# Performance work log

Measured on AMD Instinct MI355X. Metric: run time of the kernel, lower is better.

The kernel has to match this reference:

```python
import jax, jax.numpy as jnp
import numpy as np

# dimensions
B, NQ, D, H, L, KT, KF = 4, 8192, 256, 8, 4, 2, 2
K = KT * KF
DH = D // H
SPATIAL = np.array([[64, 64], [32, 32], [16, 16], [8, 8]], dtype=np.int32)  # (H_l, W_l)
_sizes = SPATIAL[:, 0] * SPATIAL[:, 1]
LSI = np.concatenate([[0], np.cumsum(_sizes)[:-1]]).astype(np.int32)
NV = int(_sizes.sum())


def setup_inputs() -> dict:
    key = jax.random.key(0)
    ks = jax.random.split(key, 12)
    s = 0.02  # small weight scale keeps tanh in linear region like the zero-init original
    # biases per _reset_parameters: +-0.5 grid for offsets, level-specialization for level_weights
    b_time = jnp.asarray(np.tile(np.linspace(-0.5, 0.5, KT), H * L).astype(np.float32))
    b_freq = jnp.asarray(np.tile(np.linspace(-0.5, 0.5, KF).astype(np.float32), H * L))
    lvl_bias = np.zeros((H, L), dtype=np.float32)
    hpl = max(1, H // L)
    for lvl in range(L):
        lvl_bias[lvl * hpl:min(lvl * hpl + hpl, H), lvl] = 1.0
    return dict(
        query=jax.random.normal(ks[0], (B, NQ, D), jnp.float32),
        reference_points=jax.random.uniform(ks[1], (B, NQ, L, 2), jnp.float32),
        value=jax.random.normal(ks[2], (B, NV, D), jnp.float32),
        spatial_shapes=jnp.asarray(SPATIAL),
        level_start_index=jnp.asarray(LSI),
        W_time=jax.random.normal(ks[3], (D, H * L * KT), jnp.float32) * s,
        b_time=b_time,
        W_freq=jax.random.normal(ks[4], (D, H * L * KF), jnp.float32) * s,
        b_freq=b_freq,
        W_lvl=jax.random.normal(ks[5], (D, H * L), jnp.float32) * s,
        b_lvl=jnp.asarray(lvl_bias.reshape(-1)),
        W_pt=jax.random.normal(ks[6], (D, H * L * K), jnp.float32) * s,
        b_pt=jnp.zeros((H * L * K,), jnp.float32),
        W_v=jax.random.normal(ks[7], (D, D), jnp.float32) * (1.0 / np.sqrt(D)),
        b_v=jnp.zeros((D,), jnp.float32),
        W_o=jax.random.normal(ks[8], (D, D), jnp.float32) * (1.0 / np.sqrt(D)),
        b_o=jnp.zeros((D,), jnp.float32),
    )


def _bilinear(vlev, gx, gy, Hl, Wl):
    # vlev: [B,H,Hl*Wl,DH]; gx,gy: [B,H,NQ,K] normalized grid coords in [-1,1]
    # F.grid_sample(align_corners=False, padding_mode='zeros') semantics
    x = (gx + 1.0) * (Wl * 0.5) - 0.5
    y = (gy + 1.0) * (Hl * 0.5) - 0.5
    x0 = jnp.floor(x)
    y0 = jnp.floor(y)
    wx1 = x - x0
    wy1 = y - y0
    x0i = x0.astype(jnp.int32)
    y0i = y0.astype(jnp.int32)

    def gather(xi, yi, w):
        valid = (xi >= 0) & (xi < Wl) & (yi >= 0) & (yi < Hl)
        idx = jnp.clip(yi, 0, Hl - 1) * Wl + jnp.clip(xi, 0, Wl - 1)
        b, h, nq, k = idx.shape
        v = jnp.take_along_axis(vlev, idx.reshape(b, h, nq * k)[..., None], axis=2)
        v = v.reshape(b, h, nq, k, DH)
        return v * (w * valid)[..., None]

    return (gather(x0i, y0i, (1.0 - wx1) * (1.0 - wy1))
            + gather(x0i + 1, y0i, wx1 * (1.0 - wy1))
            + gather(x0i, y0i + 1, (1.0 - wx1) * wy1)
            + gather(x0i + 1, y0i + 1, wx1 * wy1))


def _forward(query, reference_points, value, W_time, b_time, W_freq, b_freq,
             W_lvl, b_lvl, W_pt, b_pt, W_v, b_v, W_o, b_o,
             spatial_shapes, level_start_index):
    ss = np.asarray(spatial_shapes)
    lsi = np.asarray(level_start_index)
    # predicted separable offsets (offset_scale = 1.0)
    t_off = jnp.tanh(query @ W_time + b_time).reshape(B, NQ, H, L, KT)
    f_off = jnp.tanh(query @ W_freq + b_freq).reshape(B, NQ, H, L, KF)
    # square grid: outer product of time (x) and freq (y) offsets -> K = KT*KF points
    off = jnp.stack([
        jnp.broadcast_to(t_off[..., :, None], (B, NQ, H, L, KT, KF)),
        jnp.broadcast_to(f_off[..., None, :], (B, NQ, H, L, KT, KF)),
    ], axis=-1).reshape(B, NQ, H, L, K, 2)
    # normalizer: (W_l, H_l) per level
    norm = jnp.stack([spatial_shapes[:, 1], spatial_shapes[:, 0]], axis=-1).astype(jnp.float32)
    loc = reference_points[:, :, None, :, None, :] + off / norm[None, None, None, :, None, :]
    loc = jnp.clip(loc, 0.0, 1.0)
    grid = 2.0 * loc - 1.0  # [B,NQ,H,L,K,2], last dim = (x, y)
    # attention weights: softmax over levels times softmax over points
    lw = jax.nn.softmax((query @ W_lvl + b_lvl).reshape(B, NQ, H, L), axis=-1)
    pw = jax.nn.softmax((query @ W_pt + b_pt).reshape(B, NQ, H, L, K), axis=-1)
    attn = lw[..., None] * pw  # [B,NQ,H,L,K]
    v = (value @ W_v + b_v).reshape(B, NV, H, DH)
    out = jnp.zeros((B, NQ, H, DH), jnp.float32)
    for lid in range(L):
        Hl, Wl = int(ss[lid, 0]), int(ss[lid, 1])
        start = int(lsi[lid])
        vlev = v[:, start:start + Hl * Wl].transpose(0, 2, 1, 3)  # [B,H,S_l,DH]
        gx = grid[:, :, :, lid, :, 0].transpose(0, 2, 1, 3)  # [B,H,NQ,K]
        gy = grid[:, :, :, lid, :, 1].transpose(0, 2, 1, 3)
        sampled = _bilinear(vlev, gx, gy, Hl, Wl)  # [B,H,NQ,K,DH]
        a = attn[:, :, :, lid, :].transpose(0, 2, 1, 3)  # [B,H,NQ,K]
        out = out + jnp.einsum('bhqkd,bhqk->bqhd', sampled, a)
    out = out.reshape(B, NQ, D)
    return out @ W_o + b_o


def reference(query, reference_points, value, spatial_shapes, level_start_index,
              W_time, b_time, W_freq, b_freq, W_lvl, b_lvl, W_pt, b_pt,
              W_v, b_v, W_o, b_o):
    return _forward(query, reference_points, value, W_time, b_time, W_freq, b_freq,
                    W_lvl, b_lvl, W_pt, b_pt, W_v, b_v, W_o, b_o,
                    spatial_shapes, level_start_index)
```

## Files before the change

### kernel.cpp

```cpp
#include <hip/hip_runtime.h>
#include <math.h>

#define B_  4
#define NQ_ 8192
#define D_  256
#define H_  8
#define L_  4
#define K_  4
#define DH_ 32
#define NV_ 5440

#define SLAB_ 5936

typedef short bf16x8 __attribute__((ext_vector_type(8)));
typedef float f32x4  __attribute__((ext_vector_type(4)));
typedef float f32x8  __attribute__((ext_vector_type(8)));
typedef unsigned short u16x8 __attribute__((ext_vector_type(8)));

__device__ __forceinline__ ushort f2bf(float f) {
    union { float f; unsigned u; } v; v.f = f;
    return (ushort)((v.u + 0x7FFF + ((v.u >> 16) & 1)) >> 16);
}
__device__ __forceinline__ float bf2f(ushort u) {
    union { unsigned u; float f; } v; v.u = ((unsigned)u) << 16;
    return v.f;
}
__device__ __forceinline__ void gld16(const void* g, void* l) {
    __builtin_amdgcn_global_load_lds(
        (const __attribute__((address_space(1))) unsigned int*)g,
        (__attribute__((address_space(3))) unsigned int*)l, 16, 0, 0);
}

__global__ __launch_bounds__(256) void k_prep(const float* __restrict__ Wv,
                                              const float* __restrict__ Wo,
                                              const float* __restrict__ Wt,
                                              const float* __restrict__ Wf,
                                              const float* __restrict__ Wlv,
                                              const float* __restrict__ Wp,
                                              uint4* __restrict__ vzero,
                                              ushort* __restrict__ Wvt,
                                              ushort* __restrict__ Wot,
                                              ushort* __restrict__ Wqt) {
    const int bk = blockIdx.x;
    const int t  = threadIdx.x;
    if (bk < 2968) {
        vzero[(size_t)bk * 256 + t] = make_uint4(0, 0, 0, 0);
    } else if (bk < 3480) {
        const float* in; ushort* out; int n;
        if (bk < 3224) { in = Wv; out = Wvt; n = bk - 2968; }
        else           { in = Wo; out = Wot; n = bk - 3224; }
        out[n * 256 + t] = f2bf(in[t * 256 + n]);
    } else {
        const int n = bk - 3480;
        float v;
        if (n < 64)       v = Wt[t * 64 + n];
        else if (n < 128) v = Wf[t * 64 + (n - 64)];
        else if (n < 160) v = Wlv[t * 32 + (n - 128)];
        else              v = Wp[t * 128 + (n - 160)];
        Wqt[n * 256 + t] = f2bf(v);
    }
}

template<int MODE, int AF32>
__global__ __launch_bounds__(256) void k_gemm(const void* __restrict__ Ap,
                                              const ushort* __restrict__ Bt,
                                              const float* __restrict__ bias,
                                              void* __restrict__ Cp) {
    __shared__ __align__(16) ushort As[2][128 * 32];
    __shared__ __align__(16) ushort Bs[2][128 * 32];
    const int m0   = blockIdx.x * 128;
    const int n0   = blockIdx.y * 128;
    const int t    = threadIdx.x;
    const int w    = t >> 6;
    const int lane = t & 63;
    const int wm   = (w >> 1) * 64;
    const int wn   = (w & 1) * 64;
    const int lm   = lane & 15;
    const int quad = lane >> 4;

    float4 areg[4];

    auto stageB = [&](int buf, int kc) {
        #pragma unroll
        for (int i = 0; i < 2; ++i) {
            const int c0 = (i * 4 + w) * 64;
            const int c  = c0 + lane;
            const int row = c >> 2, ko = (c & 3) * 8;
            gld16(&Bt[(size_t)(n0 + row) * 256 + kc + ko],
                  (ushort*)&Bs[buf][0] + (size_t)c0 * 8);
        }
    };
    auto stageA16 = [&](int buf, int kc) {
        const ushort* A = (const ushort*)Ap;
        #pragma unroll
        for (int i = 0; i < 2; ++i) {
            const int c0 = (i * 4 + w) * 64;
            const int c  = c0 + lane;
            const int row = c >> 2, ko = (c & 3) * 8;
            gld16(&A[(size_t)(m0 + row) * 256 + kc + ko],
                  (ushort*)&As[buf][0] + (size_t)c0 * 8);
        }
    };
    auto loadA32 = [&](int kc) {
        const float* A = (const float*)Ap;
        #pragma unroll
        for (int i = 0; i < 4; ++i) {
            const int c = t + i * 256;
            const int row = c >> 3, ko = (c & 7) * 4;
            areg[i] = *(const float4*)&A[(size_t)(m0 + row) * 256 + kc + ko];
        }
    };
    auto writeA32 = [&](int buf) {
        #pragma unroll
        for (int i = 0; i < 4; ++i) {
            const int c = t + i * 256;
            const int row = c >> 3, ko = (c & 7) * 4;
            ushort4 u;
            u.x = f2bf(areg[i].x); u.y = f2bf(areg[i].y);
            u.z = f2bf(areg[i].z); u.w = f2bf(areg[i].w);
            *(ushort4*)&As[buf][row * 32 + ko] = u;
        }
    };

    f32x4 acc[4][4];
    #pragma unroll
    for (int i = 0; i < 4; ++i)
        #pragma unroll
        for (int j = 0; j < 4; ++j)
            acc[i][j] = (f32x4)(0.f);

    if (AF32) { loadA32(0); writeA32(0); }
    else      { stageA16(0, 0); }
    stageB(0, 0);
    __syncthreads();

    int cur = 0;
    for (int kc = 0; kc < 256; kc += 32) {
        const int nxt = cur ^ 1;
        bf16x8 af[4], bfr[4];
        #pragma unroll
        for (int mf = 0; mf < 4; ++mf)
            af[mf] = *(const bf16x8*)&As[cur][(wm + mf * 16 + lm) * 32 + quad * 8];
        #pragma unroll
        for (int nf = 0; nf < 4; ++nf)
            bfr[nf] = *(const bf16x8*)&Bs[cur][(wn + nf * 16 + lm) * 32 + quad * 8];
        if (kc + 32 < 256) {
            if (AF32) loadA32(kc + 32);
            else      stageA16(nxt, kc + 32);
            stageB(nxt, kc + 32);
        }
        #pragma unroll
        for (int mf = 0; mf < 4; ++mf)
            #pragma unroll
            for (int nf = 0; nf < 4; ++nf)
                acc[mf][nf] = __builtin_amdgcn_mfma_f32_16x16x32_bf16(
                    af[mf], bfr[nf], acc[mf][nf], 0, 0, 0);
        if (kc + 32 < 256) {
            if (AF32) writeA32(nxt);
            __syncthreads();
        }
        cur = nxt;
    }

    #pragma unroll
    for (int mf = 0; mf < 4; ++mf) {
        #pragma unroll
        for (int nf = 0; nf < 4; ++nf) {
            const f32x4 a = acc[mf][nf];
            const int col   = n0 + wn + nf * 16 + lm;
            const int rbase = m0 + wm + mf * 16 + quad * 4;
            #pragma unroll
            for (int r = 0; r < 4; ++r) {
                const int row = rbase + r;
                const float v = a[r];
                if (MODE == 0) {
                    ((float*)Cp)[(size_t)row * 256 + col] = v + bias[col];
                } else {
                    const int b = row / NV_, s = row - b * NV_;
                    const int h = col >> 5, dh = col & 31;
                    const int l = (s >= 5376) ? 3 : (s >= 5120) ? 2 : (s >= 4096) ? 1 : 0;
                    const int lsi_[4] = {0, 4096, 5120, 5376};
                    const int po_[4]  = {0, 4356, 5512, 5836};
                    const int o  = s - lsi_[l];
                    const int Wl = 64 >> l;
                    const int y  = o >> (6 - l);
                    const int x  = o & (Wl - 1);
                    const int prow = po_[l] + (y + 1) * (Wl + 2) + (x + 1);
                    ((ushort*)Cp)[(((size_t)(b * H_ + h)) * SLAB_ + prow) * 32 + dh] =
                        f2bf(v + bias[col]);
                }
            }
        }
    }
}

__global__ __launch_bounds__(256) void k_qproj(const float* __restrict__ query,
                                               const ushort* __restrict__ Wqt,
                                               const float* __restrict__ refpts,
                                               const float* __restrict__ bt,
                                               const float* __restrict__ bfq,
                                               const float* __restrict__ blv,
                                               const float* __restrict__ bp,
                                               float* __restrict__ params) {
    __shared__ __align__(16) char smem[45056];
    ushort* As0 = (ushort*)smem;
    ushort* Bs0 = (ushort*)(smem + 8192);
    float*  ep  = (float*)smem;

    const int m0   = blockIdx.x * 64;
    const int t    = threadIdx.x;
    const int w    = t >> 6;
    const int lane = t & 63;
    const int wm   = (w >> 1) * 32;
    const int wn   = (w & 1) * 144;
    const int lm   = lane & 15;
    const int quad = lane >> 4;

    float4 areg[2];

    auto stageB = [&](int buf, int kc) {
        ushort* B = Bs0 + buf * 9216;
        #pragma unroll
        for (int i = 0; i < 5; ++i) {
            const int cb = i * 4 + w;
            if (cb < 18) {
                const int c0 = cb * 64;
                const int c  = c0 + lane;
                const int row = c >> 2, ko = (c & 3) * 8;
                gld16(&Wqt[(size_t)row * 256 + kc + ko], B + (size_t)c0 * 8);
            }
        }
    };
    auto loadA = [&](int kc) {
        #pragma unroll
        for (int i = 0; i < 2; ++i) {
            const int c = t + i * 256;
            const int row = c >> 3, ko = (c & 7) * 4;
            areg[i] = *(const float4*)&query[(size_t)(m0 + row) * 256 + kc + ko];
        }
    };
    auto writeA = [&](int buf) {
        ushort* A = As0 + buf * 2048;
        #pragma unroll
        for (int i = 0; i < 2; ++i) {
            const int c = t + i * 256;
            const int row = c >> 3, ko = (c & 7) * 4;
            ushort4 u;
            u.x = f2bf(areg[i].x); u.y = f2bf(areg[i].y);
            u.z = f2bf(areg[i].z); u.w = f2bf(areg[i].w);
            *(ushort4*)&A[row * 32 + ko] = u;
        }
    };

    f32x4 acc[2][9];
    #pragma unroll
    for (int i = 0; i < 2; ++i)
        #pragma unroll
        for (int j = 0; j < 9; ++j)
            acc[i][j] = (f32x4)(0.f);

    loadA(0); writeA(0);
    stageB(0, 0);
    __syncthreads();

    int cur = 0;
    for (int kc = 0; kc < 256; kc += 32) {
        const int nxt = cur ^ 1;
        const ushort* Ac = As0 + cur * 2048;
        const ushort* Bc = Bs0 + cur * 9216;
        bf16x8 af[2], bfr[9];
        #pragma unroll
        for (int mf = 0; mf < 2; ++mf)
            af[mf] = *(const bf16x8*)&Ac[(wm + mf * 16 + lm) * 32 + quad * 8];
        #pragma unroll
        for (int nf = 0; nf < 9; ++nf)
            bfr[nf] = *(const bf16x8*)&Bc[(wn + nf * 16 + lm) * 32 + quad * 8];
        if (kc + 32 < 256) {
            loadA(kc + 32);
            stageB(nxt, kc + 32);
        }
        #pragma unroll
        for (int mf = 0; mf < 2; ++mf)
            #pragma unroll
            for (int nf = 0; nf < 9; ++nf)
                acc[mf][nf] = __builtin_amdgcn_mfma_f32_16x16x32_bf16(
                    af[mf], bfr[nf], acc[mf][nf], 0, 0, 0);
        if (kc + 32 < 256) {
            writeA(nxt);
            __syncthreads();
        }
        cur = nxt;
    }

    #pragma unroll
    for (int ph = 0; ph < 2; ++ph) {
        __syncthreads();
        if ((w >> 1) == ph) {
            #pragma unroll
            for (int mf = 0; mf < 2; ++mf)
                #pragma unroll
                for (int nf = 0; nf < 9; ++nf)
                    #pragma unroll
                    for (int r = 0; r < 4; ++r)
                        ep[(mf * 16 + quad * 4 + r) * 296 + wn + nf * 16 + lm]
                            = acc[mf][nf][r];
        }
        __syncthreads();
        #pragma unroll
        for (int it = 0; it < 4; ++it) {
            const int item = t + it * 256;
            const int qr = item >> 5;
            const int hl = item & 31;
            const int h = hl >> 2, l = hl & 3;
            const int qg = m0 + ph * 32 + qr;
            const float* lgr = &ep[qr * 296];

            const float tA = tanhf(lgr[hl * 2 + 0] + bt[hl * 2 + 0]);
            const float tB = tanhf(lgr[hl * 2 + 1] + bt[hl * 2 + 1]);
            const float fA = tanhf(lgr[64 + hl * 2 + 0] + bfq[hl * 2 + 0]);
            const float fB = tanhf(lgr[64 + hl * 2 + 1] + bfq[hl * 2 + 1]);

            const float l0 = lgr[128 + h * 4 + 0] + blv[h * 4 + 0];
            const float l1 = lgr[128 + h * 4 + 1] + blv[h * 4 + 1];
            const float l2 = lgr[128 + h * 4 + 2] + blv[h * 4 + 2];
            const float l3 = lgr[128 + h * 4 + 3] + blv[h * 4 + 3];
            const float lmx = fmaxf(fmaxf(l0, l1), fmaxf(l2, l3));
            const float e0 = __expf(l0 - lmx), e1 = __expf(l1 - lmx);
            const float e2 = __expf(l2 - lmx), e3 = __expf(l3 - lmx);
            const float lsum = e0 + e1 + e2 + e3;
            const float lwv = ((l == 0) ? e0 : (l == 1) ? e1 : (l == 2) ? e2 : e3) / lsum;

            const float p0 = lgr[160 + hl * 4 + 0] + bp[hl * 4 + 0];
            const float p1 = lgr[160 + hl * 4 + 1] + bp[hl * 4 + 1];
            const float p2 = lgr[160 + hl * 4 + 2] + bp[hl * 4 + 2];
            const float p3 = lgr[160 + hl * 4 + 3] + bp[hl * 4 + 3];
            const float pmx = fmaxf(fmaxf(p0, p1), fmaxf(p2, p3));
            const float q0e = __expf(p0 - pmx), q1e = __expf(p1 - pmx);
            const float q2e = __expf(p2 - pmx), q3e = __expf(p3 - pmx);
            const float inv = lwv / (q0e + q1e + q2e + q3e);

            const float rx = refpts[((size_t)qg * L_ + l) * 2 + 0];
            const float ry = refpts[((size_t)qg * L_ + l) * 2 + 1];
            const float Wlf = (float)(64 >> l);
            const float Hlf = (float)(64 >> l);
            const float xA = fminf(fmaxf(rx + tA / Wlf, 0.f), 1.f) * Wlf - 0.5f;
            const float xB = fminf(fmaxf(rx + tB / Wlf, 0.f), 1.f) * Wlf - 0.5f;
            const float yA = fminf(fmaxf(ry + fA / Hlf, 0.f), 1.f) * Hlf - 0.5f;
            const float yB = fminf(fmaxf(ry + fB / Hlf, 0.f), 1.f) * Hlf - 0.5f;

            float* pp = params + (size_t)qg * 256 + hl * 8;
            pp[0] = q0e * inv; pp[1] = q1e * inv; pp[2] = q2e * inv; pp[3] = q3e * inv;
            pp[4] = xA; pp[5] = xB; pp[6] = yA; pp[7] = yB;
        }
    }
}

__global__ __launch_bounds__(256) void k_sample(const ushort* __restrict__ vperm,
                                                const float* __restrict__ params,
                                                ushort* __restrict__ mid) {
    __shared__ float pm[8][264];
    const int fid = blockIdx.x;
    const int b   = (fid & 7) >> 1;
    const int q0  = (((fid >> 3) << 1) | (fid & 1)) * 8;
    const int t   = threadIdx.x;
    const int ql  = t >> 5;
    const int sub = t & 31;
    const int h   = sub >> 2;
    const int dh8 = sub & 3;

    for (int i = t; i < 8 * 256; i += 256) {
        const int q = i >> 8, c = i & 255;
        pm[q][(c >> 5) * 33 + (c & 31)] = params[((size_t)(b * NQ_ + q0 + q)) * 256 + c];
    }
    __syncthreads();

    const ushort* vb = vperm + ((size_t)(b * H_ + h)) * SLAB_ * 32 + dh8 * 8;
    const int po_[4] = {0, 4356, 5512, 5836};

    f32x8 acc = (f32x8)(0.f);
    #pragma unroll
    for (int l = 0; l < L_; ++l) {
        const int W2 = (64 >> l) + 2;
        const ushort* vl = vb + (size_t)po_[l] * 32;
        const float* p  = &pm[ql][h * 33 + l * 8];
        const float a0 = p[0], a1 = p[1], a2 = p[2], a3 = p[3];
        const float xA = p[4], xB = p[5], yA = p[6], yB = p[7];
        const float xa0 = floorf(xA), xb0 = floorf(xB);
        const float ya0 = floorf(yA), yb0 = floorf(yB);
        const float fxa = xA - xa0, fxb = xB - xb0;
        const float fya = yA - ya0, fyb = yB - yb0;
        const int pxa = (int)xa0 + 1, pxb = (int)xb0 + 1;
        const int pya = (int)ya0 + 1, pyb = (int)yb0 + 1;
        #pragma unroll
        for (int k = 0; k < 4; ++k) {
            const int   px = (k & 2) ? pxb : pxa;
            const int   py = (k & 1) ? pyb : pya;
            const float fx = (k & 2) ? fxb : fxa;
            const float fy = (k & 1) ? fyb : fya;
            const float ak = (k == 0) ? a0 : (k == 1) ? a1 : (k == 2) ? a2 : a3;
            const ushort* cp = vl + (size_t)(py * W2 + px) * 32;
            const u16x8 u00 = *(const u16x8*)cp;
            const u16x8 u10 = *(const u16x8*)(cp + 32);
            const u16x8 u01 = *(const u16x8*)(cp + W2 * 32);
            const u16x8 u11 = *(const u16x8*)(cp + (W2 + 1) * 32);
            const float gx = 1.f - fx, gy = 1.f - fy;
            const float w00 = ak * gx * gy, w10 = ak * fx * gy;
            const float w01 = ak * gx * fy, w11 = ak * fx * fy;
            #pragma unroll
            for (int e = 0; e < 8; ++e)
                acc[e] += bf2f(u00[e]) * w00 + bf2f(u10[e]) * w10
                        + bf2f(u01[e]) * w01 + bf2f(u11[e]) * w11;
        }
    }
    u16x8 o;
    #pragma unroll
    for (int e = 0; e < 8; ++e) o[e] = f2bf(acc[e]);
    *(u16x8*)&mid[((size_t)(b * NQ_ + q0 + ql)) * 256 + sub * 8] = o;
}

extern "C" void kernel_launch(void* const* d_in, const int* in_sizes, int n_in,
                              void* d_out, int out_size, void* d_ws, size_t ws_size,
                              hipStream_t stream) {
    const float* query = (const float*)d_in[0];
    const float* refp  = (const float*)d_in[1];
    const float* value = (const float*)d_in[2];
    const float* Wt = (const float*)d_in[5];
    const float* bt = (const float*)d_in[6];
    const float* Wf = (const float*)d_in[7];
    const float* bf = (const float*)d_in[8];
    const float* Wl = (const float*)d_in[9];
    const float* bl = (const float*)d_in[10];
    const float* Wp = (const float*)d_in[11];
    const float* bp = (const float*)d_in[12];
    const float* Wv = (const float*)d_in[13];
    const float* bv = (const float*)d_in[14];
    const float* Wo = (const float*)d_in[15];
    const float* bo = (const float*)d_in[16];

    char* wsb = (char*)d_ws;
    ushort* vperm  = (ushort*)wsb;
    float*  params = (float*)(wsb + 12156928);
    ushort* midb   = (ushort*)(wsb + 45711360);
    ushort* Wvt    = (ushort*)(wsb + 62488576);
    ushort* Wot    = (ushort*)(wsb + 62619648);
    ushort* Wqt    = (ushort*)(wsb + 62750720);

    k_prep<<<3768, 256, 0, stream>>>(Wv, Wo, Wt, Wf, Wl, Wp,
                                     (uint4*)vperm, Wvt, Wot, Wqt);
    k_gemm<1, 1><<<dim3(170, 2), 256, 0, stream>>>(value, Wvt, bv, vperm);
    k_qproj<<<512, 256, 0, stream>>>(query, Wqt, refp, bt, bf, bl, bp, params);
    k_sample<<<dim3(NQ_ / 8 * B_), 256, 0, stream>>>(vperm, params, midb);
    k_gemm<0, 0><<<dim3(256, 2), 256, 0, stream>>>(midb, Wot, bo, (float*)d_out);
}
```

Before: 222.4 us.

## Fuse value and query projections into one launch; zero only slab borders

Merges the value projection GEMM, the query projection/param kernel and a new border-zeroing role into a single heterogeneous launch selected by block index. The full memset of the padded value slab in the prep kernel is replaced by writing zeros only to the one-element border ring of each padded level, since the interior is overwritten by the projection. This removes a kernel launch, lets the two independent projections share the GPU concurrently, and cuts the zero-fill traffic. It relies on the border enumeration exactly covering every padded cell the sampler can read, and the fused kernel's occupancy is now bounded by the larger shared-memory footprint.

```diff
diff --git a/kernel.cpp b/kernel.cpp
--- a/kernel.cpp
+++ b/kernel.cpp
@@ -37,21 +37,18 @@
                                               const float* __restrict__ Wf,
                                               const float* __restrict__ Wlv,
                                               const float* __restrict__ Wp,
-                                              uint4* __restrict__ vzero,
                                               ushort* __restrict__ Wvt,
                                               ushort* __restrict__ Wot,
                                               ushort* __restrict__ Wqt) {
     const int bk = blockIdx.x;
     const int t  = threadIdx.x;
-    if (bk < 2968) {
-        vzero[(size_t)bk * 256 + t] = make_uint4(0, 0, 0, 0);
-    } else if (bk < 3480) {
+    if (bk < 512) {
         const float* in; ushort* out; int n;
-        if (bk < 3224) { in = Wv; out = Wvt; n = bk - 2968; }
-        else           { in = Wo; out = Wot; n = bk - 3224; }
+        if (bk < 256) { in = Wv; out = Wvt; n = bk; }
+        else          { in = Wo; out = Wot; n = bk - 256; }
         out[n * 256 + t] = f2bf(in[t * 256 + n]);
     } else {
-        const int n = bk - 3480;
+        const int n = bk - 512;
         float v;
         if (n < 64)       v = Wt[t * 64 + n];
         else if (n < 128) v = Wf[t * 64 + (n - 64)];
@@ -61,11 +58,339 @@
     }
 }
 
-template<int MODE, int AF32>
-__global__ __launch_bounds__(256) void k_gemm(const void* __restrict__ Ap,
-                                              const ushort* __restrict__ Bt,
-                                              const float* __restrict__ bias,
-                                              void* __restrict__ Cp) {
+__device__ __forceinline__ void vproj_role(char* smem, int fid,
+                                           const float* __restrict__ value,
+                                           const ushort* __restrict__ Wvt,
+                                           const float* __restrict__ bv,
+                                           ushort* __restrict__ vperm) {
+    ushort* As0 = (ushort*)smem;
+    ushort* Bs0 = (ushort*)(smem + 16384);
+    const int m0   = (fid % 170) * 128;
+    const int n0   = (fid / 170) * 128;
+    const int t    = threadIdx.x;
+    const int w    = t >> 6;
+    const int lane = t & 63;
+    const int wm   = (w >> 1) * 64;
+    const int wn   = (w & 1) * 64;
+    const int lm   = lane & 15;
+    const int quad = lane >> 4;
+
+    float4 areg[4];
+
+    auto stageB = [&](int buf, int kc) {
+        ushort* B = Bs0 + buf * 4096;
+        #pragma unroll
+        for (int i = 0; i < 2; ++i) {
+            const int c0 = (i * 4 + w) * 64;
+            const int c  = c0 + lane;
+            const int row = c >> 2, ko = (c & 3) * 8;
+            gld16(&Wvt[(size_t)(n0 + row) * 256 + kc + ko], B + (size_t)c0 * 8);
+        }
+    };
+    auto loadA = [&](int kc) {
+        #pragma unroll
+        for (int i = 0; i < 4; ++i) {
+            const int c = t + i * 256;
+            const int row = c >> 3, ko = (c & 7) * 4;
+            areg[i] = *(const float4*)&value[(size_t)(m0 + row) * 256 + kc + ko];
+        }
+    };
+    auto writeA = [&](int buf) {
+        ushort* A = As0 + buf * 4096;
+        #pragma unroll
+        for (int i = 0; i < 4; ++i) {
+            const int c = t + i * 256;
+            const int row = c >> 3, ko = (c & 7) * 4;
+            ushort4 u;
+            u.x = f2bf(areg[i].x); u.y = f2bf(areg[i].y);
+            u.z = f2bf(areg[i].z); u.w = f2bf(areg[i].w);
+            *(ushort4*)&A[row * 32 + ko] = u;
+        }
+    };
+
+    f32x4 acc[4][4];
+    #pragma unroll
+    for (int i = 0; i < 4; ++i)
+        #pragma unroll
+        for (int j = 0; j < 4; ++j)
+            acc[i][j] = (f32x4)(0.f);
+
+    loadA(0); writeA(0);
+    stageB(0, 0);
+    __syncthreads();
+
+    int cur = 0;
+    for (int kc = 0; kc < 256; kc += 32) {
+        const int nxt = cur ^ 1;
+        const ushort* Ac = As0 + cur * 4096;
+        const ushort* Bc = Bs0 + cur * 4096;
+        bf16x8 af[4], bfr[4];
+        #pragma unroll
+        for (int mf = 0; mf < 4; ++mf)
+            af[mf] = *(const bf16x8*)&Ac[(wm + mf * 16 + lm) * 32 + quad * 8];
+        #pragma unroll
+        for (int nf = 0; nf < 4; ++nf)
+            bfr[nf] = *(const bf16x8*)&Bc[(wn + nf * 16 + lm) * 32 + quad * 8];
+        if (kc + 32 < 256) {
+            loadA(kc + 32);
+            stageB(nxt, kc + 32);
+        }
+        #pragma unroll
+        for (int mf = 0; mf < 4; ++mf)
+            #pragma unroll
+            for (int nf = 0; nf < 4; ++nf)
+                acc[mf][nf] = __builtin_amdgcn_mfma_f32_16x16x32_bf16(
+                    af[mf], bfr[nf], acc[mf][nf], 0, 0, 0);
+        if (kc + 32 < 256) {
+            writeA(nxt);
+            __syncthreads();
+        }
+        cur = nxt;
+    }
+
+    #pragma unroll
+    for (int mf = 0; mf < 4; ++mf) {
+        #pragma unroll
+        for (int nf = 0; nf < 4; ++nf) {
+            const f32x4 a = acc[mf][nf];
+            const int col   = n0 + wn + nf * 16 + lm;
+            const int rbase = m0 + wm + mf * 16 + quad * 4;
+            #pragma unroll
+            for (int r = 0; r < 4; ++r) {
+                const int row = rbase + r;
+                const float v = a[r];
+                const int b = row / NV_, s = row - b * NV_;
+                const int h = col >> 5, dh = col & 31;
+                const int l = (s >= 5376) ? 3 : (s >= 5120) ? 2 : (s >= 4096) ? 1 : 0;
+                const int lsi_[4] = {0, 4096, 5120, 5376};
+                const int po_[4]  = {0, 4356, 5512, 5836};
+                const int o  = s - lsi_[l];
+                const int Wl = 64 >> l;
+                const int y  = o >> (6 - l);
+                const int x  = o & (Wl - 1);
+                const int prow = po_[l] + (y + 1) * (Wl + 2) + (x + 1);
+                vperm[(((size_t)(b * H_ + h)) * SLAB_ + prow) * 32 + dh] =
+                    f2bf(v + bv[col]);
+            }
+        }
+    }
+}
+
+__device__ __forceinline__ void qproj_role(char* smem, int fid,
+                                           const float* __restrict__ query,
+                                           const ushort* __restrict__ Wqt,
+                                           const float* __restrict__ refpts,
+                                           const float* __restrict__ bt,
+                                           const float* __restrict__ bfq,
+                                           const float* __restrict__ blv,
+                                           const float* __restrict__ bp,
+                                           float* __restrict__ params) {
+    ushort* As0 = (ushort*)smem;
+    ushort* Bs0 = (ushort*)(smem + 8192);
+    float*  ep  = (float*)smem;
+
+    const int m0   = fid * 64;
+    const int t    = threadIdx.x;
+    const int w    = t >> 6;
+    const int lane = t & 63;
+    const int wm   = (w >> 1) * 32;
+    const int wn   = (w & 1) * 144;
+    const int lm   = lane & 15;
+    const int quad = lane >> 4;
+
+    float4 areg[2];
+
+    auto stageB = [&](int buf, int kc) {
+        ushort* B = Bs0 + buf * 9216;
+        #pragma unroll
+        for (int i = 0; i < 5; ++i) {
+            const int cb = i * 4 + w;
+            if (cb < 18) {
+                const int c0 = cb * 64;
+                const int c  = c0 + lane;
+                const int row = c >> 2, ko = (c & 3) * 8;
+                gld16(&Wqt[(size_t)row * 256 + kc + ko], B + (size_t)c0 * 8);
+            }
+        }
+    };
+    auto loadA = [&](int kc) {
+        #pragma unroll
+        for (int i = 0; i < 2; ++i) {
+            const int c = t + i * 256;
+            const int row = c >> 3, ko = (c & 7) * 4;
+            areg[i] = *(const float4*)&query[(size_t)(m0 + row) * 256 + kc + ko];
+        }
+    };
+    auto writeA = [&](int buf) {
+        ushort* A = As0 + buf * 2048;
+        #pragma unroll
+        for (int i = 0; i < 2; ++i) {
+            const int c = t + i * 256;
+            const int row = c >> 3, ko = (c & 7) * 4;
+            ushort4 u;
+            u.x = f2bf(areg[i].x); u.y = f2bf(areg[i].y);
+            u.z = f2bf(areg[i].z); u.w = f2bf(areg[i].w);
+            *(ushort4*)&A[row * 32 + ko] = u;
+        }
+    };
+
+    f32x4 acc[2][9];
+    #pragma unroll
+    for (int i = 0; i < 2; ++i)
+        #pragma unroll
+        for (int j = 0; j < 9; ++j)
+            acc[i][j] = (f32x4)(0.f);
+
+    loadA(0); writeA(0);
+    stageB(0, 0);
+    __syncthreads();
+
+    int cur = 0;
+    for (int kc = 0; kc < 256; kc += 32) {
+        const int nxt = cur ^ 1;
+        const ushort* Ac = As0 + cur * 2048;
+        const ushort* Bc = Bs0 + cur * 9216;
+        bf16x8 af[2], bfr[9];
+        #pragma unroll
+        for (int mf = 0; mf < 2; ++mf)
+            af[mf] = *(const bf16x8*)&Ac[(wm + mf * 16 + lm) * 32 + quad * 8];
+        #pragma unroll
+        for (int nf = 0; nf < 9; ++nf)
+            bfr[nf] = *(const bf16x8*)&Bc[(wn + nf * 16 + lm) * 32 + quad * 8];
+        if (kc + 32 < 256) {
+            loadA(kc + 32);
+            stageB(nxt, kc + 32);
+        }
+        #pragma unroll
+        for (int mf = 0; mf < 2; ++mf)
+            #pragma unroll
+            for (int nf = 0; nf < 9; ++nf)
+                acc[mf][nf] = __builtin_amdgcn_mfma_f32_16x16x32_bf16(
+                    af[mf], bfr[nf], acc[mf][nf], 0, 0, 0);
+        if (kc + 32 < 256) {
+            writeA(nxt);
+            __syncthreads();
+        }
+        cur = nxt;
+    }
+
+    #pragma unroll
+    for (int ph = 0; ph < 2; ++ph) {
+        __syncthreads();
+        if ((w >> 1) == ph) {
+            #pragma unroll
+            for (int mf = 0; mf < 2; ++mf)
+                #pragma unroll
+                for (int nf = 0; nf < 9; ++nf)
+                    #pragma unroll
+                    for (int r = 0; r < 4; ++r)
+                        ep[(mf * 16 + quad * 4 + r) * 296 + wn + nf * 16 + lm]
+                            = acc[mf][nf][r];
+        }
+        __syncthreads();
+        #pragma unroll
+        for (int it = 0; it < 4; ++it) {
+            const int item = t + it * 256;
+            const int qr = item >> 5;
+            const int hl = item & 31;
+            const int h = hl >> 2, l = hl & 3;
+            const int qg = m0 + ph * 32 + qr;
+            const float* lgr = &ep[qr * 296];
+
+            const float tA = tanhf(lgr[hl * 2 + 0] + bt[hl * 2 + 0]);
+            const float tB = tanhf(lgr[hl * 2 + 1] + bt[hl * 2 + 1]);
+            const float fA = tanhf(lgr[64 + hl * 2 + 0] + bfq[hl * 2 + 0]);
+            const float fB = tanhf(lgr[64 + hl * 2 + 1] + bfq[hl * 2 + 1]);
+
+            const float l0 = lgr[128 + h * 4 + 0] + blv[h * 4 + 0];
+            const float l1 = lgr[128 + h * 4 + 1] + blv[h * 4 + 1];
+            const float l2 = lgr[128 + h * 4 + 2] + blv[h * 4 + 2];
+            const float l3 = lgr[128 + h * 4 + 3] + blv[h * 4 + 3];
+            const float lmx = fmaxf(fmaxf(l0, l1), fmaxf(l2, l3));
+            const float e0 = __expf(l0 - lmx), e1 = __expf(l1 - lmx);
+            const float e2 = __expf(l2 - lmx), e3 = __expf(l3 - lmx);
+            const float lsum = e0 + e1 + e2 + e3;
+            const float lwv = ((l == 0) ? e0 : (l == 1) ? e1 : (l == 2) ? e2 : e3) / lsum;
+
+            const float p0 = lgr[160 + hl * 4 + 0] + bp[hl * 4 + 0];
+            const float p1 = lgr[160 + hl * 4 + 1] + bp[hl * 4 + 1];
+            const float p2 = lgr[160 + hl * 4 + 2] + bp[hl * 4 + 2];
+            const float p3 = lgr[160 + hl * 4 + 3] + bp[hl * 4 + 3];
+            const float pmx = fmaxf(fmaxf(p0, p1), fmaxf(p2, p3));
+            const float q0e = __expf(p0 - pmx), q1e = __expf(p1 - pmx);
+            const float q2e = __expf(p2 - pmx), q3e = __expf(p3 - pmx);
+            const float inv = lwv / (q0e + q1e + q2e + q3e);
+
+            const float rx = refpts[((size_t)qg * L_ + l) * 2 + 0];
+            const float ry = refpts[((size_t)qg * L_ + l) * 2 + 1];
+            const float Wlf = (float)(64 >> l);
+            const float Hlf = (float)(64 >> l);
+            const float xA = fminf(fmaxf(rx + tA / Wlf, 0.f), 1.f) * Wlf - 0.5f;
+            const float xB = fminf(fmaxf(rx + tB / Wlf, 0.f), 1.f) * Wlf - 0.5f;
+            const float yA = fminf(fmaxf(ry + fA / Hlf, 0.f), 1.f) * Hlf - 0.5f;
+            const float yB = fminf(fmaxf(ry + fB / Hlf, 0.f), 1.f) * Hlf - 0.5f;
+
+            float* pp = params + (size_t)qg * 256 + hl * 8;
+            pp[0] = q0e * inv; pp[1] = q1e * inv; pp[2] = q2e * inv; pp[3] = q3e * inv;
+            pp[4] = xA; pp[5] = xB; pp[6] = yA; pp[7] = yB;
+        }
+    }
+}
+
+__device__ __forceinline__ void border_role(int fid, ushort* __restrict__ vperm) {
+    const int t = threadIdx.x;
+    const int p = fid * 256 + t;
+    const int bh = p / 496;
+    int e = p - bh * 496;
+    int l = 0;
+    if (e >= 460)      { l = 3; e -= 460; }
+    else if (e >= 392) { l = 2; e -= 392; }
+    else if (e >= 260) { l = 1; e -= 260; }
+    const int po_[4] = {0, 4356, 5512, 5836};
+    const int W2 = (64 >> l) + 2;
+    int row, col;
+    if (e < 2 * W2) {
+        row = (e < W2) ? 0 : (W2 - 1);
+        col = (e < W2) ? e : (e - W2);
+    } else {
+        const int e2 = e - 2 * W2;
+        row = 1 + (e2 >> 1);
+        col = (e2 & 1) ? (W2 - 1) : 0;
+    }
+    uint4* dst = (uint4*)&vperm[((size_t)bh * SLAB_ + po_[l] + row * W2 + col) * 32];
+    dst[0] = make_uint4(0, 0, 0, 0);
+    dst[1] = make_uint4(0, 0, 0, 0);
+    dst[2] = make_uint4(0, 0, 0, 0);
+    dst[3] = make_uint4(0, 0, 0, 0);
+}
+
+__global__ __launch_bounds__(256) void k_fused(const float* __restrict__ value,
+                                               const ushort* __restrict__ Wvt,
+                                               const float* __restrict__ bv,
+                                               ushort* __restrict__ vperm,
+                                               const float* __restrict__ query,
+                                               const ushort* __restrict__ Wqt,
+                                               const float* __restrict__ refpts,
+                                               const float* __restrict__ bt,
+                                               const float* __restrict__ bfq,
+                                               const float* __restrict__ blv,
+                                               const float* __restrict__ bp,
+                                               float* __restrict__ params) {
+    __shared__ __align__(16) char smem[45056];
+    const int fid = blockIdx.x;
+    if (fid < 340) {
+        vproj_role(smem, fid, value, Wvt, bv, vperm);
+    } else if (fid < 852) {
+        qproj_role(smem, fid - 340, query, Wqt, refpts, bt, bfq, blv, bp, params);
+    } else {
+        border_role(fid - 852, vperm);
+    }
+}
+
+__global__ __launch_bounds__(256) void k_ogemm(const ushort* __restrict__ A,
+                                               const ushort* __restrict__ Bt,
+                                               const float* __restrict__ bias,
+                                               float* __restrict__ Cp) {
     __shared__ __align__(16) ushort As[2][128 * 32];
     __shared__ __align__(16) ushort Bs[2][128 * 32];
     const int m0   = blockIdx.x * 128;
@@ -78,47 +403,13 @@
     const int lm   = lane & 15;
     const int quad = lane >> 4;
 
-    float4 areg[4];
-
-    auto stageB = [&](int buf, int kc) {
+    auto stage = [&](ushort* dst, const ushort* src, int row0, int kc) {
         #pragma unroll
         for (int i = 0; i < 2; ++i) {
             const int c0 = (i * 4 + w) * 64;
             const int c  = c0 + lane;
             const int row = c >> 2, ko = (c & 3) * 8;
-            gld16(&Bt[(size_t)(n0 + row) * 256 + kc + ko],
-                  (ushort*)&Bs[buf][0] + (size_t)c0 * 8);
-        }
-    };
-    auto stageA16 = [&](int buf, int kc) {
-        const ushort* A = (const ushort*)Ap;
-        #pragma unroll
-        for (int i = 0; i < 2; ++i) {
-            const int c0 = (i * 4 + w) * 64;
-            const int c  = c0 + lane;
-            const int row = c >> 2, ko = (c & 3) * 8;
-            gld16(&A[(size_t)(m0 + row) * 256 + kc + ko],
-                  (ushort*)&As[buf][0] + (size_t)c0 * 8);
-        }
-    };
-    auto loadA32 = [&](int kc) {
-        const float* A = (const float*)Ap;
-        #pragma unroll
-        for (int i = 0; i < 4; ++i) {
-            const int c = t + i * 256;
-            const int row = c >> 3, ko = (c & 7) * 4;
-            areg[i] = *(const float4*)&A[(size_t)(m0 + row) * 256 + kc + ko];
-        }
-    };
-    auto writeA32 = [&](int buf) {
-        #pragma unroll
-        for (int i = 0; i < 4; ++i) {
-            const int c = t + i * 256;
-            const int row = c >> 3, ko = (c & 7) * 4;
-            ushort4 u;
-            u.x = f2bf(areg[i].x); u.y = f2bf(areg[i].y);
-            u.z = f2bf(areg[i].z); u.w = f2bf(areg[i].w);
-            *(ushort4*)&As[buf][row * 32 + ko] = u;
+            gld16(&src[(size_t)(row0 + row) * 256 + kc + ko], dst + (size_t)c0 * 8);
         }
     };
 
@@ -129,9 +420,8 @@
         for (int j = 0; j < 4; ++j)
             acc[i][j] = (f32x4)(0.f);
 
-    if (AF32) { loadA32(0); writeA32(0); }
-    else      { stageA16(0, 0); }
-    stageB(0, 0);
+    stage(&As[0][0], A, m0, 0);
+    stage(&Bs[0][0], Bt, n0, 0);
     __syncthreads();
 
     int cur = 0;
@@ -145,9 +435,8 @@
         for (int nf = 0; nf < 4; ++nf)
             bfr[nf] = *(const bf16x8*)&Bs[cur][(wn + nf * 16 + lm) * 32 + quad * 8];
         if (kc + 32 < 256) {
-            if (AF32) loadA32(kc + 32);
-            else      stageA16(nxt, kc + 32);
-            stageB(nxt, kc + 32);
+            stage(&As[nxt][0], A, m0, kc + 32);
+            stage(&Bs[nxt][0], Bt, n0, kc + 32);
         }
         #pragma unroll
         for (int mf = 0; mf < 4; ++mf)
@@ -155,10 +444,7 @@
             for (int nf = 0; nf < 4; ++nf)
                 acc[mf][nf] = __builtin_amdgcn_mfma_f32_16x16x32_bf16(
                     af[mf], bfr[nf], acc[mf][nf], 0, 0, 0);
-        if (kc + 32 < 256) {
-            if (AF32) writeA32(nxt);
-            __syncthreads();
-        }
+        if (kc + 32 < 256) __syncthreads();
         cur = nxt;
     }
 
@@ -170,187 +456,8 @@
             const int col   = n0 + wn + nf * 16 + lm;
             const int rbase = m0 + wm + mf * 16 + quad * 4;
             #pragma unroll
-            for (int r = 0; r < 4; ++r) {
-                const int row = rbase + r;
-                const float v = a[r];
-                if (MODE == 0) {
-                    ((float*)Cp)[(size_t)row * 256 + col] = v + bias[col];
-                } else {
-                    const int b = row / NV_, s = row - b * NV_;
-                    const int h = col >> 5, dh = col & 31;
-                    const int l = (s >= 5376) ? 3 : (s >= 5120) ? 2 : (s >= 4096) ? 1 : 0;
-                    const int lsi_[4] = {0, 4096, 5120, 5376};
-                    const int po_[4]  = {0, 4356, 5512, 5836};
-                    const int o  = s - lsi_[l];
-                    const int Wl = 64 >> l;
-                    const int y  = o >> (6 - l);
-                    const int x  = o & (Wl - 1);
-                    const int prow = po_[l] + (y + 1) * (Wl + 2) + (x + 1);
-                    ((ushort*)Cp)[(((size_t)(b * H_ + h)) * SLAB_ + prow) * 32 + dh] =
-                        f2bf(v + bias[col]);
-                }
-            }
-        }
-    }
-}
-
-__global__ __launch_bounds__(256) void k_qproj(const float* __restrict__ query,
-                                               const ushort* __restrict__ Wqt,
-                                               const float* __restrict__ refpts,
-                                               const float* __restrict__ bt,
-                                               const float* __restrict__ bfq,
-                                               const float* __restrict__ blv,
-                                               const float* __restrict__ bp,
-                                               float* __restrict__ params) {
-    __shared__ __align__(16) char smem[45056];
-    ushort* As0 = (ushort*)smem;
-    ushort* Bs0 = (ushort*)(smem + 8192);
-    float*  ep  = (float*)smem;
-
-    const int m0   = blockIdx.x * 64;
-    const int t    = threadIdx.x;
-    const int w    = t >> 6;
-    const int lane = t & 63;
-    const int wm   = (w >> 1) * 32;
-    const int wn   = (w & 1) * 144;
-    const int lm   = lane & 15;
-    const int quad = lane >> 4;
-
-    float4 areg[2];
-
-    auto stageB = [&](int buf, int kc) {
-        ushort* B = Bs0 + buf * 9216;
-        #pragma unroll
-        for (int i = 0; i < 5; ++i) {
-            const int cb = i * 4 + w;
-            if (cb < 18) {
-                const int c0 = cb * 64;
-                const int c  = c0 + lane;
-                const int row = c >> 2, ko = (c & 3) * 8;
-                gld16(&Wqt[(size_t)row * 256 + kc + ko], B + (size_t)c0 * 8);
-            }
-        }
-    };
-    auto loadA = [&](int kc) {
-        #pragma unroll
-        for (int i = 0; i < 2; ++i) {
-            const int c = t + i * 256;
-            const int row = c >> 3, ko = (c & 7) * 4;
-            areg[i] = *(const float4*)&query[(size_t)(m0 + row) * 256 + kc + ko];
-        }
-    };
-    auto writeA = [&](int buf) {
-        ushort* A = As0 + buf * 2048;
-        #pragma unroll
-        for (int i = 0; i < 2; ++i) {
-            const int c = t + i * 256;
-            const int row = c >> 3, ko = (c & 7) * 4;
-            ushort4 u;
-            u.x = f2bf(areg[i].x); u.y = f2bf(areg[i].y);
-            u.z = f2bf(areg[i].z); u.w = f2bf(areg[i].w);
-            *(ushort4*)&A[row * 32 + ko] = u;
-        }
-    };
-
-    f32x4 acc[2][9];
-    #pragma unroll
-    for (int i = 0; i < 2; ++i)
-        #pragma unroll
-        for (int j = 0; j < 9; ++j)
-            acc[i][j] = (f32x4)(0.f);
-
-    loadA(0); writeA(0);
-    stageB(0, 0);
-    __syncthreads();
-
-    int cur = 0;
-    for (int kc = 0; kc < 256; kc += 32) {
-        const int nxt = cur ^ 1;
-        const ushort* Ac = As0 + cur * 2048;
-        const ushort* Bc = Bs0 + cur * 9216;
-        bf16x8 af[2], bfr[9];
-        #pragma unroll
-        for (int mf = 0; mf < 2; ++mf)
-            af[mf] = *(const bf16x8*)&Ac[(wm + mf * 16 + lm) * 32 + quad * 8];
-        #pragma unroll
-        for (int nf = 0; nf < 9; ++nf)
-            bfr[nf] = *(const bf16x8*)&Bc[(wn + nf * 16 + lm) * 32 + quad * 8];
-        if (kc + 32 < 256) {
-            loadA(kc + 32);
-            stageB(nxt, kc + 32);
-        }
-        #pragma unroll
-        for (int mf = 0; mf < 2; ++mf)
-            #pragma unroll
-            for (int nf = 0; nf < 9; ++nf)
-                acc[mf][nf] = __builtin_amdgcn_mfma_f32_16x16x32_bf16(
-                    af[mf], bfr[nf], acc[mf][nf], 0, 0, 0);
-        if (kc + 32 < 256) {
-            writeA(nxt);
-            __syncthreads();
-        }
-        cur = nxt;
-    }
-
-    #pragma unroll
-    for (int ph = 0; ph < 2; ++ph) {
-        __syncthreads();
-        if ((w >> 1) == ph) {
-            #pragma unroll
-            for (int mf = 0; mf < 2; ++mf)
-                #pragma unroll
-                for (int nf = 0; nf < 9; ++nf)
-                    #pragma unroll
-                    for (int r = 0; r < 4; ++r)
-                        ep[(mf * 16 + quad * 4 + r) * 296 + wn + nf * 16 + lm]
-                            = acc[mf][nf][r];
-        }
-        __syncthreads();
-        #pragma unroll
-        for (int it = 0; it < 4; ++it) {
-            const int item = t + it * 256;
-            const int qr = item >> 5;
-            const int hl = item & 31;
-            const int h = hl >> 2, l = hl & 3;
-            const int qg = m0 + ph * 32 + qr;
-            const float* lgr = &ep[qr * 296];
-
-            const float tA = tanhf(lgr[hl * 2 + 0] + bt[hl * 2 + 0]);
-            const float tB = tanhf(lgr[hl * 2 + 1] + bt[hl * 2 + 1]);
-            const float fA = tanhf(lgr[64 + hl * 2 + 0] + bfq[hl * 2 + 0]);
-            const float fB = tanhf(lgr[64 + hl * 2 + 1] + bfq[hl * 2 + 1]);
-
-            const float l0 = lgr[128 + h * 4 + 0] + blv[h * 4 + 0];
-            const float l1 = lgr[128 + h * 4 + 1] + blv[h * 4 + 1];
-            const float l2 = lgr[128 + h * 4 + 2] + blv[h * 4 + 2];
-            const float l3 = lgr[128 + h * 4 + 3] + blv[h * 4 + 3];
-            const float lmx = fmaxf(fmaxf(l0, l1), fmaxf(l2, l3));
-            const float e0 = __expf(l0 - lmx), e1 = __expf(l1 - lmx);
-            const float e2 = __expf(l2 - lmx), e3 = __expf(l3 - lmx);
-            const float lsum = e0 + e1 + e2 + e3;
-            const float lwv = ((l == 0) ? e0 : (l == 1) ? e1 : (l == 2) ? e2 : e3) / lsum;
-
-            const float p0 = lgr[160 + hl * 4 + 0] + bp[hl * 4 + 0];
-            const float p1 = lgr[160 + hl * 4 + 1] + bp[hl * 4 + 1];
-            const float p2 = lgr[160 + hl * 4 + 2] + bp[hl * 4 + 2];
-            const float p3 = lgr[160 + hl * 4 + 3] + bp[hl * 4 + 3];
-            const float pmx = fmaxf(fmaxf(p0, p1), fmaxf(p2, p3));
-            const float q0e = __expf(p0 - pmx), q1e = __expf(p1 - pmx);
-            const float q2e = __expf(p2 - pmx), q3e = __expf(p3 - pmx);
-            const float inv = lwv / (q0e + q1e + q2e + q3e);
-
-            const float rx = refpts[((size_t)qg * L_ + l) * 2 + 0];
-            const float ry = refpts[((size_t)qg * L_ + l) * 2 + 1];
-            const float Wlf = (float)(64 >> l);
-            const float Hlf = (float)(64 >> l);
-            const float xA = fminf(fmaxf(rx + tA / Wlf, 0.f), 1.f) * Wlf - 0.5f;
-            const float xB = fminf(fmaxf(rx + tB / Wlf, 0.f), 1.f) * Wlf - 0.5f;
-            const float yA = fminf(fmaxf(ry + fA / Hlf, 0.f), 1.f) * Hlf - 0.5f;
-            const float yB = fminf(fmaxf(ry + fB / Hlf, 0.f), 1.f) * Hlf - 0.5f;
-
-            float* pp = params + (size_t)qg * 256 + hl * 8;
-            pp[0] = q0e * inv; pp[1] = q1e * inv; pp[2] = q2e * inv; pp[3] = q3e * inv;
-            pp[4] = xA; pp[5] = xB; pp[6] = yA; pp[7] = yB;
+            for (int r = 0; r < 4; ++r)
+                Cp[(size_t)(rbase + r) * 256 + col] = a[r] + bias[col];
         }
     }
 }
@@ -445,10 +552,9 @@
     ushort* Wot    = (ushort*)(wsb + 62619648);
     ushort* Wqt    = (ushort*)(wsb + 62750720);
 
-    k_prep<<<3768, 256, 0, stream>>>(Wv, Wo, Wt, Wf, Wl, Wp,
-                                     (uint4*)vperm, Wvt, Wot, Wqt);
-    k_gemm<1, 1><<<dim3(170, 2), 256, 0, stream>>>(value, Wvt, bv, vperm);
-    k_qproj<<<512, 256, 0, stream>>>(query, Wqt, refp, bt, bf, bl, bp, params);
+    k_prep<<<800, 256, 0, stream>>>(Wv, Wo, Wt, Wf, Wl, Wp, Wvt, Wot, Wqt);
+    k_fused<<<914, 256, 0, stream>>>(value, Wvt, bv, vperm,
+                                     query, Wqt, refp, bt, bf, bl, bp, params);
     k_sample<<<dim3(NQ_ / 8 * B_), 256, 0, stream>>>(vperm, params, midb);
-    k_gemm<0, 0><<<dim3(256, 2), 256, 0, stream>>>(midb, Wot, bo, (float*)d_out);
-}
+    k_ogemm<<<dim3(256, 2), 256, 0, stream>>>(midb, Wot, bo, (float*)d_out);
+}
```

Measured after the change: 220.8 us. About the same (-0.7%).
